# Optimization experiments

Measured on AMD Instinct MI355X. Metric: run time of the kernel, lower is better.

## Reference

```python
import jax, jax.numpy as jnp
import numpy as np

NF4 = jnp.array([-1.0, -0.6961928009986877, -0.5250730514526367, -0.39491748809814453,
                 -0.28444138169288635, -0.18477343022823334, -0.09105003625154495, 0.0,
                 0.07958029955625534, 0.16093020141124725, 0.24611230194568634,
                 0.33791524171829224, 0.44070982933044434, 0.5626170039176941,
                 0.7229568362236023, 1.0], dtype=jnp.float32)

IN_FEATURES = 2048
OUT_FEATURES = 8192
BLOCK_SIZE = 64


def setup_inputs() -> dict:
    key = jax.random.key(0)
    k1, k2, k3, k4 = jax.random.split(key, 4)
    n_elems = OUT_FEATURES * IN_FEATURES
    n_blocks = n_elems // BLOCK_SIZE
    x = jax.random.normal(k1, (2, 2048, IN_FEATURES), dtype=jnp.float32)
    q = jax.random.randint(k2, (n_elems,), 0, 16, dtype=jnp.int32)
    scale = jax.random.uniform(k3, (n_blocks,), dtype=jnp.float32)  # absmax >= 0
    bias = jax.random.normal(k4, (OUT_FEATURES,), dtype=jnp.float32)
    return {"x": x, "q": q, "scale": scale, "bias": bias}


def reference(x, q, scale, bias):
    # Dequantize: NF4 table lookup per 4-bit code, per-block absmax scale.
    n_blocks = scale.shape[0]
    codes = q.reshape(n_blocks, BLOCK_SIZE)                  # (n_blocks, 64)
    w = NF4[codes] * scale[:, None]                          # (n_blocks, 64)
    w = w.reshape(OUT_FEATURES, IN_FEATURES)                 # (out, in)
    # F.linear: y = x @ W^T + b
    return jnp.einsum('bsi,oi->bso', x, w) + bias
```

## Files before the change

### kernel.cpp

```cpp
#include <hip/hip_runtime.h>
#include <stdint.h>

#define GM 4096
#define GN 8192
#define GK 2048

typedef float f32x4 __attribute__((ext_vector_type(4)));
typedef __bf16 bf16x8 __attribute__((ext_vector_type(8)));

__device__ __constant__ float NF4_LUT[16] = {
    -1.0f, -0.6961928009986877f, -0.5250730514526367f, -0.39491748809814453f,
    -0.28444138169288635f, -0.18477343022823334f, -0.09105003625154495f, 0.0f,
    0.07958029955625534f, 0.16093020141124725f, 0.24611230194568634f,
    0.33791524171829224f, 0.44070982933044434f, 0.5626170039176941f,
    0.7229568362236023f, 1.0f};

__device__ __forceinline__ unsigned short f32_to_bf16_rne(float f) {
  union { float f; uint32_t u; } v;
  v.f = f;
  uint32_t lsb = (v.u >> 16) & 1u;
  v.u += 0x7fffu + lsb;
  return (unsigned short)(v.u >> 16);
}

__global__ void __launch_bounds__(256) dequant_nf4_kernel(
    const int* __restrict__ q, const float* __restrict__ scale,
    unsigned short* __restrict__ w) {
  __shared__ float lut[16];
  if (threadIdx.x < 16) lut[threadIdx.x] = NF4_LUT[threadIdx.x];
  __syncthreads();
  int t = blockIdx.x * 256 + threadIdx.x;
  const int4* q4 = reinterpret_cast<const int4*>(q);
  int4 c0 = q4[2 * t];
  int4 c1 = q4[2 * t + 1];
  float s = scale[t >> 3];
  int codes[8] = {c0.x, c0.y, c0.z, c0.w, c1.x, c1.y, c1.z, c1.w};
  union { unsigned short u[8]; int4 v; } r;
#pragma unroll
  for (int j = 0; j < 8; ++j)
    r.u[j] = f32_to_bf16_rne(lut[codes[j] & 15] * s);
  reinterpret_cast<int4*>(w)[t] = r.v;
}

__global__ void __launch_bounds__(256) cvt_f32_bf16_kernel(
    const float* __restrict__ x, unsigned short* __restrict__ xb) {
  int t = blockIdx.x * 256 + threadIdx.x;
  const float4* x4 = reinterpret_cast<const float4*>(x);
  float4 a = x4[2 * t];
  float4 b = x4[2 * t + 1];
  union { unsigned short u[8]; int4 v; } r;
  r.u[0] = f32_to_bf16_rne(a.x); r.u[1] = f32_to_bf16_rne(a.y);
  r.u[2] = f32_to_bf16_rne(a.z); r.u[3] = f32_to_bf16_rne(a.w);
  r.u[4] = f32_to_bf16_rne(b.x); r.u[5] = f32_to_bf16_rne(b.y);
  r.u[6] = f32_to_bf16_rne(b.z); r.u[7] = f32_to_bf16_rne(b.w);
  reinterpret_cast<int4*>(xb)[t] = r.v;
}

#define AS1(p) ((const __attribute__((address_space(1))) void*)(p))
#define AS3(p) ((__attribute__((address_space(3))) void*)(p))
#define VM6() asm volatile("s_waitcnt vmcnt(6)" ::: "memory")
#define FENCE() asm volatile("" ::: "memory")
#define BAR() do { FENCE(); __builtin_amdgcn_s_barrier(); FENCE(); } while (0)

__global__ void __launch_bounds__(512, 1) gemm_8phase_kernel(
    const unsigned short* __restrict__ A,
    const unsigned short* __restrict__ B,
    const float* __restrict__ bias, float* __restrict__ C) {
  constexpr int BK = 64;
  constexpr int NV = 64;
  __shared__ __align__(16) unsigned short As[2 * 256 * 64];
  __shared__ __align__(16) unsigned short Bs[2 * 256 * 64];

  int bid = blockIdx.x;
  int swz = (bid & 7) * 32 + (bid >> 3);
  int brow = (swz & 15) * 256;
  int pair = swz >> 4;
  int bcol0 = pair * 512;

  int tid = threadIdx.x;
  int lane = tid & 63;
  int wave = tid >> 6;
  int wr = wave >> 2;
  int wc = wave & 3;
  int fr = lane & 15;
  int slot = lane >> 4;
  int swc = (slot << 4) ^ ((fr & 7) << 4);

  const unsigned short* Abase = A + (size_t)brow * GK;
  const unsigned short* Bbase0 = B + (size_t)bcol0 * GK;
  const unsigned short* Bbase1 = Bbase0 + (size_t)256 * GK;

  int arow = (wr * 64 + fr) * 128;
  int brw = (wc * 32 + fr) * 128;

  f32x4 acc[8][4] = {};
  bf16x8 a0[2][4][2], a1[2][4][2], b0[2][2][2], b1[2][2][2];

  auto ldA = [&](int buf, int qm, int m, int kk) -> bf16x8 {
    int off = buf * 32768 + qm * 16384 + m * 2048 + arow + (swc ^ (kk << 6));
    return *reinterpret_cast<const bf16x8*>((const char*)As + off);
  };
  auto ldB = [&](int buf, int qn, int n, int kk) -> bf16x8 {
    int off = buf * 32768 + qn * 16384 + n * 2048 + brw + (swc ^ (kk << 6));
    return *reinterpret_cast<const bf16x8*>((const char*)Bs + off);
  };
  auto stage = [&](const unsigned short* gtile, unsigned short* lds, int buf,
                   int h, int kt) {
#pragma unroll
    for (int i = 0; i < 2; ++i) {
      int L = h * 16384 + i * 8192 + tid * 16;
      int s = L ^ (((L >> 7) & 7) << 4);
      __builtin_amdgcn_global_load_lds(
          AS1(gtile + (size_t)(s >> 7) * GK + kt + ((s & 127) >> 1)),
          AS3((char*)lds + buf * 32768 + L), 16, 0, 0);
    }
  };
  auto RD_A1 = [&](int p) {
#pragma unroll
    for (int m = 0; m < 4; ++m)
#pragma unroll
      for (int kk = 0; kk < 2; ++kk) a1[p][m][kk] = ldA(p, 1, m, kk);
  };
  auto RD_B1 = [&](int p) {
#pragma unroll
    for (int n = 0; n < 2; ++n)
#pragma unroll
      for (int kk = 0; kk < 2; ++kk) b1[p][n][kk] = ldB(p, 1, n, kk);
  };
  auto RD_A0B0 = [&](int p) {
#pragma unroll
    for (int m = 0; m < 4; ++m)
#pragma unroll
      for (int kk = 0; kk < 2; ++kk) a0[p][m][kk] = ldA(p, 0, m, kk);
#pragma unroll
    for (int n = 0; n < 2; ++n)
#pragma unroll
      for (int kk = 0; kk < 2; ++kk) b0[p][n][kk] = ldB(p, 0, n, kk);
  };
  auto Q1 = [&](int p) {
    __builtin_amdgcn_s_setprio(1);
#pragma unroll
    for (int m = 0; m < 4; ++m)
#pragma unroll
      for (int n = 0; n < 2; ++n)
#pragma unroll
        for (int kk = 0; kk < 2; ++kk)
          acc[m][n] = __builtin_amdgcn_mfma_f32_16x16x32_bf16(
              a0[p][m][kk], b0[p][n][kk], acc[m][n], 0, 0, 0);
    __builtin_amdgcn_s_setprio(0);
  };
  auto Q2 = [&](int p) {
    __builtin_amdgcn_s_setprio(1);
#pragma unroll
    for (int m = 0; m < 4; ++m)
#pragma unroll
      for (int n = 0; n < 2; ++n)
#pragma unroll
        for (int kk = 0; kk < 2; ++kk)
          acc[4 + m][n] = __builtin_amdgcn_mfma_f32_16x16x32_bf16(
              a1[p][m][kk], b0[p][n][kk], acc[4 + m][n], 0, 0, 0);
    __builtin_amdgcn_s_setprio(0);
  };
  auto Q3 = [&](int p) {
    __builtin_amdgcn_s_setprio(1);
#pragma unroll
    for (int m = 0; m < 4; ++m)
#pragma unroll
      for (int n = 0; n < 2; ++n)
#pragma unroll
        for (int kk = 0; kk < 2; ++kk)
          acc[4 + m][2 + n] = __builtin_amdgcn_mfma_f32_16x16x32_bf16(
              a1[p][m][kk], b1[p][n][kk], acc[4 + m][2 + n], 0, 0, 0);
    __builtin_amdgcn_s_setprio(0);
  };
  auto Q4 = [&](int p) {
    __builtin_amdgcn_s_setprio(1);
#pragma unroll
    for (int m = 0; m < 4; ++m)
#pragma unroll
      for (int n = 0; n < 2; ++n)
#pragma unroll
        for (int kk = 0; kk < 2; ++kk)
          acc[m][2 + n] = __builtin_amdgcn_mfma_f32_16x16x32_bf16(
              a0[p][m][kk], b1[p][n][kk], acc[m][2 + n], 0, 0, 0);
    __builtin_amdgcn_s_setprio(0);
  };
  auto flush = [&](int bc) {
    float bv[4];
#pragma unroll
    for (int n = 0; n < 4; ++n)
      bv[n] = bias[bc + (n >> 1) * 128 + wc * 32 + (n & 1) * 16 + fr];
#pragma unroll
    for (int m = 0; m < 8; ++m) {
      int grow0 = brow + (m >> 2) * 128 + wr * 64 + (m & 3) * 16 + slot * 4;
#pragma unroll
      for (int n = 0; n < 4; ++n) {
        int gcol = bc + (n >> 1) * 128 + wc * 32 + (n & 1) * 16 + fr;
#pragma unroll
        for (int r = 0; r < 4; ++r)
          C[(size_t)(grow0 + r) * GN + gcol] = acc[m][n][r] + bv[n];
      }
    }
  };
  auto iter = [&](int j) {
    int t1 = 2 * j + 1;
    int t2 = 2 * j + 2; if (t2 > NV - 1) t2 = NV - 1;
    int t3 = 2 * j + 3; if (t3 > NV - 1) t3 = NV - 1;
    const unsigned short* B1p = (t1 < 32) ? Bbase0 : Bbase1;
    const unsigned short* B2p = (t2 < 32) ? Bbase0 : Bbase1;
    const unsigned short* B3p = (t3 < 32) ? Bbase0 : Bbase1;
    int kt1 = (t1 & 31) * BK, kt2 = (t2 & 31) * BK, kt3 = (t3 & 31) * BK;
    RD_A1(0);
    stage(B1p, Bs, 1, 1, kt1);
    BAR();
    Q1(0);
    RD_B1(0);
    BAR();
    Q2(0);
    stage(Abase, As, 0, 0, kt2);
    stage(B2p, Bs, 0, 0, kt2);
    BAR();
    Q3(0);
    stage(Abase, As, 0, 1, kt2);
    VM6();
    BAR();
    RD_A0B0(1);
    Q4(0);
    RD_A1(1);
    stage(B2p, Bs, 0, 1, kt2);
    BAR();
    Q1(1);
    RD_B1(1);
    BAR();
    Q2(1);
    stage(Abase, As, 1, 0, kt3);
    stage(B3p, Bs, 1, 0, kt3);
    BAR();
    Q3(1);
    stage(Abase, As, 1, 1, kt3);
    VM6();
    BAR();
    RD_A0B0(0);
    Q4(1);
  };

  stage(Abase, As, 0, 0, 0);
  stage(Bbase0, Bs, 0, 0, 0);
  stage(Abase, As, 0, 1, 0);
  stage(Bbase0, Bs, 0, 1, 0);
  stage(Abase, As, 1, 0, BK);
  stage(Bbase0, Bs, 1, 0, BK);
  stage(Abase, As, 1, 1, BK);
  VM6();
  BAR();
  RD_A0B0(0);

#pragma unroll 1
  for (int j = 0; j < 16; ++j) iter(j);

  flush(bcol0);
#pragma unroll
  for (int m = 0; m < 8; ++m)
#pragma unroll
    for (int n = 0; n < 4; ++n)
      acc[m][n] = f32x4{0.f, 0.f, 0.f, 0.f};

#pragma unroll 1
  for (int j = 16; j < 32; ++j) iter(j);

  flush(bcol0 + 256);
}

__global__ void __launch_bounds__(256) fallback_kernel(
    const float* __restrict__ x, const int* __restrict__ q,
    const float* __restrict__ scale, const float* __restrict__ bias,
    float* __restrict__ out) {
  __shared__ float wrow[GK];
  int n = blockIdx.x;
  for (int k = threadIdx.x; k < GK; k += 256) {
    size_t idx = (size_t)n * GK + k;
    wrow[k] = NF4_LUT[q[idx] & 15] * scale[idx >> 6];
  }
  __syncthreads();
  int m = blockIdx.y * 256 + threadIdx.x;
  const float* xr = x + (size_t)m * GK;
  float acc = 0.f;
  for (int k = 0; k < GK; ++k) acc += xr[k] * wrow[k];
  out[(size_t)m * GN + n] = acc + bias[n];
}

extern "C" void kernel_launch(void* const* d_in, const int* in_sizes, int n_in,
                              void* d_out, int out_size, void* d_ws, size_t ws_size,
                              hipStream_t stream) {
  const float* x = (const float*)d_in[0];
  const int* q = (const int*)d_in[1];
  const float* scale = (const float*)d_in[2];
  const float* bias = (const float*)d_in[3];
  float* out = (float*)d_out;

  const size_t wbytes = (size_t)GN * GK * 2;
  const size_t xbytes = (size_t)GM * GK * 2;

  if (ws_size >= wbytes + xbytes) {
    unsigned short* wq = (unsigned short*)d_ws;
    unsigned short* xb = (unsigned short*)((char*)d_ws + wbytes);
    dequant_nf4_kernel<<<(GN * GK / 8) / 256, 256, 0, stream>>>(q, scale, wq);
    cvt_f32_bf16_kernel<<<(GM * GK / 8) / 256, 256, 0, stream>>>(x, xb);
    gemm_8phase_kernel<<<dim3(256), 512, 0, stream>>>(xb, wq, bias, out);
  } else {
    fallback_kernel<<<dim3(GN, GM / 256), 256, 0, stream>>>(x, q, scale, bias, out);
  }
}
```

Measured before the change: 154.2 us.

## Restructure GEMM main loop into per-tile four-quadrant schedule with fewer fragment registers

Replaces the two-tile unrolled 8-phase loop with a per-K-tile loop that loads A and B fragments for one quadrant at a time and computes four 4x2 MFMA quadrants in turn, with explicit lgkmcnt waits and barriers between phases. Fragment registers drop from double-buffered a0/a1/b0/b1 to a single a/b0/b1 set, which lowers register pressure. Global-to-LDS staging of the tile two ahead is spread across the quadrant phases, and a VM0 drain handles the tail. The schedule adds more barriers per K tile and exposes LDS read latency before each quadrant, which may cost more than the register savings recover.

```diff
diff --git a/kernel.cpp b/kernel.cpp
--- a/kernel.cpp
+++ b/kernel.cpp
@@ -59,6 +59,11 @@
 #define AS1(p) ((const __attribute__((address_space(1))) void*)(p))
 #define AS3(p) ((__attribute__((address_space(3))) void*)(p))
 #define VM6() asm volatile("s_waitcnt vmcnt(6)" ::: "memory")
+#define VM0() asm volatile("s_waitcnt vmcnt(0)" ::: "memory")
+#define VM8() asm volatile("s_waitcnt vmcnt(8)" ::: "memory")
+#define LGKM8() asm volatile("s_waitcnt lgkmcnt(8)" ::: "memory")
+#define LGKM0() do { asm volatile("s_waitcnt lgkmcnt(0)" ::: "memory"); \
+                     __builtin_amdgcn_sched_barrier(0); } while (0)
 #define FENCE() asm volatile("" ::: "memory")
 #define BAR() do { FENCE(); __builtin_amdgcn_s_barrier(); FENCE(); } while (0)
 
@@ -94,7 +99,7 @@
   int brw = (wc * 32 + fr) * 128;
 
   f32x4 acc[8][4] = {};
-  bf16x8 a0[2][4][2], a1[2][4][2], b0[2][2][2], b1[2][2][2];
+  bf16x8 a[4][2], b0[2][2], b1[2][2];
 
   auto ldA = [&](int buf, int qm, int m, int kk) -> bf16x8 {
     int off = buf * 32768 + qm * 16384 + m * 2048 + arow + (swc ^ (kk << 6));
@@ -115,29 +120,37 @@
           AS3((char*)lds + buf * 32768 + L), 16, 0, 0);
     }
   };
-  auto RD_A1 = [&](int p) {
+  auto RD_A = [&](int buf, int qm) {
 #pragma unroll
     for (int m = 0; m < 4; ++m)
 #pragma unroll
-      for (int kk = 0; kk < 2; ++kk) a1[p][m][kk] = ldA(p, 1, m, kk);
-  };
-  auto RD_B1 = [&](int p) {
+      for (int kk = 0; kk < 2; ++kk) a[m][kk] = ldA(buf, qm, m, kk);
+  };
+  auto RD_B0 = [&](int buf) {
 #pragma unroll
     for (int n = 0; n < 2; ++n)
 #pragma unroll
-      for (int kk = 0; kk < 2; ++kk) b1[p][n][kk] = ldB(p, 1, n, kk);
-  };
-  auto RD_A0B0 = [&](int p) {
+      for (int kk = 0; kk < 2; ++kk) b0[n][kk] = ldB(buf, 0, n, kk);
+  };
+  auto RD_B1 = [&](int buf) {
+#pragma unroll
+    for (int n = 0; n < 2; ++n)
+#pragma unroll
+      for (int kk = 0; kk < 2; ++kk) b1[n][kk] = ldB(buf, 1, n, kk);
+  };
+  auto QUAD0 = [&](int mb, int nb) {
+    __builtin_amdgcn_s_setprio(1);
 #pragma unroll
     for (int m = 0; m < 4; ++m)
 #pragma unroll
-      for (int kk = 0; kk < 2; ++kk) a0[p][m][kk] = ldA(p, 0, m, kk);
-#pragma unroll
-    for (int n = 0; n < 2; ++n)
-#pragma unroll
-      for (int kk = 0; kk < 2; ++kk) b0[p][n][kk] = ldB(p, 0, n, kk);
-  };
-  auto Q1 = [&](int p) {
+      for (int n = 0; n < 2; ++n)
+#pragma unroll
+        for (int kk = 0; kk < 2; ++kk)
+          acc[mb + m][nb + n] = __builtin_amdgcn_mfma_f32_16x16x32_bf16(
+              a[m][kk], b0[n][kk], acc[mb + m][nb + n], 0, 0, 0);
+    __builtin_amdgcn_s_setprio(0);
+  };
+  auto QUAD1 = [&](int mb, int nb) {
     __builtin_amdgcn_s_setprio(1);
 #pragma unroll
     for (int m = 0; m < 4; ++m)
@@ -145,44 +158,8 @@
       for (int n = 0; n < 2; ++n)
 #pragma unroll
         for (int kk = 0; kk < 2; ++kk)
-          acc[m][n] = __builtin_amdgcn_mfma_f32_16x16x32_bf16(
-              a0[p][m][kk], b0[p][n][kk], acc[m][n], 0, 0, 0);
-    __builtin_amdgcn_s_setprio(0);
-  };
-  auto Q2 = [&](int p) {
-    __builtin_amdgcn_s_setprio(1);
-#pragma unroll
-    for (int m = 0; m < 4; ++m)
-#pragma unroll
-      for (int n = 0; n < 2; ++n)
-#pragma unroll
-        for (int kk = 0; kk < 2; ++kk)
-          acc[4 + m][n] = __builtin_amdgcn_mfma_f32_16x16x32_bf16(
-              a1[p][m][kk], b0[p][n][kk], acc[4 + m][n], 0, 0, 0);
-    __builtin_amdgcn_s_setprio(0);
-  };
-  auto Q3 = [&](int p) {
-    __builtin_amdgcn_s_setprio(1);
-#pragma unroll
-    for (int m = 0; m < 4; ++m)
-#pragma unroll
-      for (int n = 0; n < 2; ++n)
-#pragma unroll
-        for (int kk = 0; kk < 2; ++kk)
-          acc[4 + m][2 + n] = __builtin_amdgcn_mfma_f32_16x16x32_bf16(
-              a1[p][m][kk], b1[p][n][kk], acc[4 + m][2 + n], 0, 0, 0);
-    __builtin_amdgcn_s_setprio(0);
-  };
-  auto Q4 = [&](int p) {
-    __builtin_amdgcn_s_setprio(1);
-#pragma unroll
-    for (int m = 0; m < 4; ++m)
-#pragma unroll
-      for (int n = 0; n < 2; ++n)
-#pragma unroll
-        for (int kk = 0; kk < 2; ++kk)
-          acc[m][2 + n] = __builtin_amdgcn_mfma_f32_16x16x32_bf16(
-              a0[p][m][kk], b1[p][n][kk], acc[m][2 + n], 0, 0, 0);
+          acc[mb + m][nb + n] = __builtin_amdgcn_mfma_f32_16x16x32_bf16(
+              a[m][kk], b1[n][kk], acc[mb + m][nb + n], 0, 0, 0);
     __builtin_amdgcn_s_setprio(0);
   };
   auto flush = [&](int bc) {
@@ -202,61 +179,51 @@
       }
     }
   };
-  auto iter = [&](int j) {
-    int t1 = 2 * j + 1;
-    int t2 = 2 * j + 2; if (t2 > NV - 1) t2 = NV - 1;
-    int t3 = 2 * j + 3; if (t3 > NV - 1) t3 = NV - 1;
-    const unsigned short* B1p = (t1 < 32) ? Bbase0 : Bbase1;
+
+  auto tile = [&](int v) {
+    int buf = v & 1;
+    int t2 = v + 2;
+    int st = (t2 < NV);
     const unsigned short* B2p = (t2 < 32) ? Bbase0 : Bbase1;
-    const unsigned short* B3p = (t3 < 32) ? Bbase0 : Bbase1;
-    int kt1 = (t1 & 31) * BK, kt2 = (t2 & 31) * BK, kt3 = (t3 & 31) * BK;
-    RD_A1(0);
-    stage(B1p, Bs, 1, 1, kt1);
-    BAR();
-    Q1(0);
-    RD_B1(0);
-    BAR();
-    Q2(0);
-    stage(Abase, As, 0, 0, kt2);
-    stage(B2p, Bs, 0, 0, kt2);
-    BAR();
-    Q3(0);
-    stage(Abase, As, 0, 1, kt2);
-    VM6();
-    BAR();
-    RD_A0B0(1);
-    Q4(0);
-    RD_A1(1);
-    stage(B2p, Bs, 0, 1, kt2);
-    BAR();
-    Q1(1);
-    RD_B1(1);
-    BAR();
-    Q2(1);
-    stage(Abase, As, 1, 0, kt3);
-    stage(B3p, Bs, 1, 0, kt3);
-    BAR();
-    Q3(1);
-    stage(Abase, As, 1, 1, kt3);
-    VM6();
-    BAR();
-    RD_A0B0(0);
-    Q4(1);
+    int kt2 = (t2 & 31) * BK;
+    RD_A(buf, 0);
+    RD_B0(buf);
+    LGKM8();
+    BAR();
+    LGKM0();
+    QUAD0(0, 0);
+    BAR();
+    RD_B1(buf);
+    if (st) stage(Abase, As, buf, 0, kt2);
+    BAR();
+    LGKM0();
+    QUAD1(0, 2);
+    BAR();
+    RD_A(buf, 1);
+    if (st) { stage(B2p, Bs, buf, 0, kt2); stage(B2p, Bs, buf, 1, kt2); }
+    BAR();
+    LGKM0();
+    QUAD1(4, 2);
+    BAR();
+    if (st) { stage(Abase, As, buf, 1, kt2); VM6(); } else { VM0(); }
+    BAR();
+    QUAD0(4, 0);
+    BAR();
   };
 
   stage(Abase, As, 0, 0, 0);
   stage(Bbase0, Bs, 0, 0, 0);
+  stage(Bbase0, Bs, 0, 1, 0);
   stage(Abase, As, 0, 1, 0);
-  stage(Bbase0, Bs, 0, 1, 0);
   stage(Abase, As, 1, 0, BK);
   stage(Bbase0, Bs, 1, 0, BK);
+  stage(Bbase0, Bs, 1, 1, BK);
   stage(Abase, As, 1, 1, BK);
-  VM6();
+  VM8();
   BAR();
-  RD_A0B0(0);
 
 #pragma unroll 1
-  for (int j = 0; j < 16; ++j) iter(j);
+  for (int v = 0; v < 32; ++v) tile(v);
 
   flush(bcol0);
 #pragma unroll
@@ -266,7 +233,7 @@
       acc[m][n] = f32x4{0.f, 0.f, 0.f, 0.f};
 
 #pragma unroll 1
-  for (int j = 16; j < 32; ++j) iter(j);
+  for (int v = 32; v < 64; ++v) tile(v);
 
   flush(bcol0 + 256);
 }
```

Result: slower. 162.3 us (+5.2%).

## Switch GEMM inner tiles from 16x16x32 to 32x32x16 bf16 MFMA

Applied to the files above, without the earlier changes.

Replaces the 16x16x32 MFMA fragments with 32x32x16 MFMA fragments, which changes the per-wave accumulator layout, the LDS fragment read addressing, the swizzle, and the output flush mapping. Larger MFMA tiles need fewer LDS fragment reads per FLOP and fewer instructions issued. In exchange, the flush stores become more scattered across rows (16 rows per lane), and the new swizzle may cause LDS bank conflicts.

```diff
diff --git a/kernel.cpp b/kernel.cpp
--- a/kernel.cpp
+++ b/kernel.cpp
@@ -6,6 +6,7 @@
 #define GK 2048
 
 typedef float f32x4 __attribute__((ext_vector_type(4)));
+typedef float f32x16 __attribute__((ext_vector_type(16)));
 typedef __bf16 bf16x8 __attribute__((ext_vector_type(8)));
 
 __device__ __constant__ float NF4_LUT[16] = {
@@ -62,7 +63,7 @@
 #define FENCE() asm volatile("" ::: "memory")
 #define BAR() do { FENCE(); __builtin_amdgcn_s_barrier(); FENCE(); } while (0)
 
-__global__ void __launch_bounds__(512, 1) gemm_8phase_kernel(
+__global__ void __launch_bounds__(512, 1) gemm_32x32_kernel(
     const unsigned short* __restrict__ A,
     const unsigned short* __restrict__ B,
     const float* __restrict__ bias, float* __restrict__ C) {
@@ -82,27 +83,21 @@
   int wave = tid >> 6;
   int wr = wave >> 2;
   int wc = wave & 3;
-  int fr = lane & 15;
-  int slot = lane >> 4;
-  int swc = (slot << 4) ^ ((fr & 7) << 4);
+  int l31 = lane & 31;
+  int hl = lane >> 5;
 
   const unsigned short* Abase = A + (size_t)brow * GK;
   const unsigned short* Bbase0 = B + (size_t)bcol0 * GK;
   const unsigned short* Bbase1 = Bbase0 + (size_t)256 * GK;
 
-  int arow = (wr * 64 + fr) * 128;
-  int brw = (wc * 32 + fr) * 128;
-
-  f32x4 acc[8][4] = {};
-  bf16x8 a0[2][4][2], a1[2][4][2], b0[2][2][2], b1[2][2][2];
-
-  auto ldA = [&](int buf, int qm, int m, int kk) -> bf16x8 {
-    int off = buf * 32768 + qm * 16384 + m * 2048 + arow + (swc ^ (kk << 6));
-    return *reinterpret_cast<const bf16x8*>((const char*)As + off);
-  };
-  auto ldB = [&](int buf, int qn, int n, int kk) -> bf16x8 {
-    int off = buf * 32768 + qn * 16384 + n * 2048 + brw + (swc ^ (kk << 6));
-    return *reinterpret_cast<const bf16x8*>((const char*)Bs + off);
+  f32x16 acc[4][2] = {};
+  bf16x8 a0[2][2][4], a1[2][2][4], b0[2][4], b1[2][4];
+
+  auto ldfrag = [&](const unsigned short* lds, int buf, int row,
+                    int ks) -> bf16x8 {
+    int g = ((ks << 1) | hl) ^ (lane & 7);
+    int off = buf * 32768 + row * 128 + (g << 4);
+    return *reinterpret_cast<const bf16x8*>((const char*)lds + off);
   };
   auto stage = [&](const unsigned short* gtile, unsigned short* lds, int buf,
                    int h, int kt) {
@@ -115,90 +110,85 @@
           AS3((char*)lds + buf * 32768 + L), 16, 0, 0);
     }
   };
+  auto RD_A0 = [&](int p) {
+#pragma unroll
+    for (int mf = 0; mf < 2; ++mf)
+#pragma unroll
+      for (int ks = 0; ks < 4; ++ks)
+        a0[p][mf][ks] = ldfrag(As, p, wr * 64 + mf * 32 + l31, ks);
+  };
   auto RD_A1 = [&](int p) {
 #pragma unroll
-    for (int m = 0; m < 4; ++m)
-#pragma unroll
-      for (int kk = 0; kk < 2; ++kk) a1[p][m][kk] = ldA(p, 1, m, kk);
+    for (int mf = 0; mf < 2; ++mf)
+#pragma unroll
+      for (int ks = 0; ks < 4; ++ks)
+        a1[p][mf][ks] = ldfrag(As, p, 128 + wr * 64 + mf * 32 + l31, ks);
+  };
+  auto RD_B0 = [&](int p) {
+#pragma unroll
+    for (int ks = 0; ks < 4; ++ks)
+      b0[p][ks] = ldfrag(Bs, p, wc * 32 + l31, ks);
   };
   auto RD_B1 = [&](int p) {
 #pragma unroll
-    for (int n = 0; n < 2; ++n)
-#pragma unroll
-      for (int kk = 0; kk < 2; ++kk) b1[p][n][kk] = ldB(p, 1, n, kk);
-  };
-  auto RD_A0B0 = [&](int p) {
-#pragma unroll
-    for (int m = 0; m < 4; ++m)
-#pragma unroll
-      for (int kk = 0; kk < 2; ++kk) a0[p][m][kk] = ldA(p, 0, m, kk);
-#pragma unroll
-    for (int n = 0; n < 2; ++n)
-#pragma unroll
-      for (int kk = 0; kk < 2; ++kk) b0[p][n][kk] = ldB(p, 0, n, kk);
+    for (int ks = 0; ks < 4; ++ks)
+      b1[p][ks] = ldfrag(Bs, p, 128 + wc * 32 + l31, ks);
   };
   auto Q1 = [&](int p) {
     __builtin_amdgcn_s_setprio(1);
 #pragma unroll
-    for (int m = 0; m < 4; ++m)
-#pragma unroll
-      for (int n = 0; n < 2; ++n)
-#pragma unroll
-        for (int kk = 0; kk < 2; ++kk)
-          acc[m][n] = __builtin_amdgcn_mfma_f32_16x16x32_bf16(
-              a0[p][m][kk], b0[p][n][kk], acc[m][n], 0, 0, 0);
+    for (int mf = 0; mf < 2; ++mf)
+#pragma unroll
+      for (int ks = 0; ks < 4; ++ks)
+        acc[mf][0] = __builtin_amdgcn_mfma_f32_32x32x16_bf16(
+            a0[p][mf][ks], b0[p][ks], acc[mf][0], 0, 0, 0);
     __builtin_amdgcn_s_setprio(0);
   };
   auto Q2 = [&](int p) {
     __builtin_amdgcn_s_setprio(1);
 #pragma unroll
-    for (int m = 0; m < 4; ++m)
-#pragma unroll
-      for (int n = 0; n < 2; ++n)
-#pragma unroll
-        for (int kk = 0; kk < 2; ++kk)
-          acc[4 + m][n] = __builtin_amdgcn_mfma_f32_16x16x32_bf16(
-              a1[p][m][kk], b0[p][n][kk], acc[4 + m][n], 0, 0, 0);
+    for (int mf = 0; mf < 2; ++mf)
+#pragma unroll
+      for (int ks = 0; ks < 4; ++ks)
+        acc[2 + mf][0] = __builtin_amdgcn_mfma_f32_32x32x16_bf16(
+            a1[p][mf][ks], b0[p][ks], acc[2 + mf][0], 0, 0, 0);
     __builtin_amdgcn_s_setprio(0);
   };
   auto Q3 = [&](int p) {
     __builtin_amdgcn_s_setprio(1);
 #pragma unroll
-    for (int m = 0; m < 4; ++m)
-#pragma unroll
-      for (int n = 0; n < 2; ++n)
-#pragma unroll
-        for (int kk = 0; kk < 2; ++kk)
-          acc[4 + m][2 + n] = __builtin_amdgcn_mfma_f32_16x16x32_bf16(
-              a1[p][m][kk], b1[p][n][kk], acc[4 + m][2 + n], 0, 0, 0);
+    for (int mf = 0; mf < 2; ++mf)
+#pragma unroll
+      for (int ks = 0; ks < 4; ++ks)
+        acc[2 + mf][1] = __builtin_amdgcn_mfma_f32_32x32x16_bf16(
+            a1[p][mf][ks], b1[p][ks], acc[2 + mf][1], 0, 0, 0);
     __builtin_amdgcn_s_setprio(0);
   };
   auto Q4 = [&](int p) {
     __builtin_amdgcn_s_setprio(1);
 #pragma unroll
-    for (int m = 0; m < 4; ++m)
-#pragma unroll
-      for (int n = 0; n < 2; ++n)
-#pragma unroll
-        for (int kk = 0; kk < 2; ++kk)
-          acc[m][2 + n] = __builtin_amdgcn_mfma_f32_16x16x32_bf16(
-              a0[p][m][kk], b1[p][n][kk], acc[m][2 + n], 0, 0, 0);
+    for (int mf = 0; mf < 2; ++mf)
+#pragma unroll
+      for (int ks = 0; ks < 4; ++ks)
+        acc[mf][1] = __builtin_amdgcn_mfma_f32_32x32x16_bf16(
+            a0[p][mf][ks], b1[p][ks], acc[mf][1], 0, 0, 0);
     __builtin_amdgcn_s_setprio(0);
   };
   auto flush = [&](int bc) {
-    float bv[4];
-#pragma unroll
-    for (int n = 0; n < 4; ++n)
-      bv[n] = bias[bc + (n >> 1) * 128 + wc * 32 + (n & 1) * 16 + fr];
-#pragma unroll
-    for (int m = 0; m < 8; ++m) {
-      int grow0 = brow + (m >> 2) * 128 + wr * 64 + (m & 3) * 16 + slot * 4;
-#pragma unroll
-      for (int n = 0; n < 4; ++n) {
-        int gcol = bc + (n >> 1) * 128 + wc * 32 + (n & 1) * 16 + fr;
-#pragma unroll
-        for (int r = 0; r < 4; ++r)
-          C[(size_t)(grow0 + r) * GN + gcol] = acc[m][n][r] + bv[n];
+    float bv[2];
+#pragma unroll
+    for (int n = 0; n < 2; ++n) bv[n] = bias[bc + n * 128 + wc * 32 + l31];
+#pragma unroll
+    for (int m = 0; m < 4; ++m) {
+      int grow = brow + (m >> 1) * 128 + wr * 64 + (m & 1) * 32 + 4 * hl;
+#pragma unroll
+      for (int n = 0; n < 2; ++n) {
+        int gcol = bc + n * 128 + wc * 32 + l31;
+#pragma unroll
+        for (int reg = 0; reg < 16; ++reg) {
+          int rif = (reg & 3) + 8 * (reg >> 2);
+          C[(size_t)(grow + rif) * GN + gcol] = acc[m][n][reg] + bv[n];
+        }
       }
     }
   };
@@ -224,7 +214,7 @@
     stage(Abase, As, 0, 1, kt2);
     VM6();
     BAR();
-    RD_A0B0(1);
+    RD_A0(1); RD_B0(1);
     Q4(0);
     RD_A1(1);
     stage(B2p, Bs, 0, 1, kt2);
@@ -240,7 +230,7 @@
     stage(Abase, As, 1, 1, kt3);
     VM6();
     BAR();
-    RD_A0B0(0);
+    RD_A0(0); RD_B0(0);
     Q4(1);
   };
 
@@ -253,17 +243,18 @@
   stage(Abase, As, 1, 1, BK);
   VM6();
   BAR();
-  RD_A0B0(0);
+  RD_A0(0); RD_B0(0);
 
 #pragma unroll 1
   for (int j = 0; j < 16; ++j) iter(j);
 
   flush(bcol0);
 #pragma unroll
-  for (int m = 0; m < 8; ++m)
-#pragma unroll
-    for (int n = 0; n < 4; ++n)
-      acc[m][n] = f32x4{0.f, 0.f, 0.f, 0.f};
+  for (int m = 0; m < 4; ++m)
+#pragma unroll
+    for (int n = 0; n < 2; ++n)
+#pragma unroll
+      for (int r = 0; r < 16; ++r) acc[m][n][r] = 0.f;
 
 #pragma unroll 1
   for (int j = 16; j < 32; ++j) iter(j);
@@ -306,7 +297,7 @@
     unsigned short* xb = (unsigned short*)((char*)d_ws + wbytes);
     dequant_nf4_kernel<<<(GN * GK / 8) / 256, 256, 0, stream>>>(q, scale, wq);
     cvt_f32_bf16_kernel<<<(GM * GK / 8) / 256, 256, 0, stream>>>(x, xb);
-    gemm_8phase_kernel<<<dim3(256), 512, 0, stream>>>(xb, wq, bias, out);
+    gemm_32x32_kernel<<<dim3(256), 512, 0, stream>>>(xb, wq, bias, out);
   } else {
     fallback_kernel<<<dim3(GN, GM / 256), 256, 0, stream>>>(x, q, scale, bias, out);
   }
```

After: 232.9 us. +51.0%, slower.
